# Performance work log

Hardware: AMD Instinct MI355X
Metric: run time of the kernel (lower is better)

## Reference

```python
import jax, jax.numpy as jnp
import numpy as np

TEMPERATURE = 1.0
K = 30
N_CELLS = 200000
LATENT = 256
BATCH = 8192

def setup_inputs() -> dict:
    key = jax.random.key(0)
    k1, k2, k3, k4 = jax.random.split(key, 4)
    z_all = jax.random.normal(k1, (N_CELLS, LATENT), dtype=jnp.float32)
    pre_knn_indices = jax.random.randint(k2, (N_CELLS, K), 0, N_CELLS, dtype=jnp.int64)
    cell_indices = jax.random.randint(k3, (BATCH,), 0, N_CELLS, dtype=jnp.int64)
    neg_indices = jax.random.randint(k4, (BATCH, K), 0, N_CELLS, dtype=jnp.int64)
    return {"z_all": z_all, "pre_knn_indices": pre_knn_indices,
            "cell_indices": cell_indices, "neg_indices": neg_indices}

def reference(z_all, pre_knn_indices, cell_indices, neg_indices):
    # z_all: (N, D); pre_knn_indices: (N, K); cell_indices: (B,); neg_indices: (B, K)
    z_i = z_all[cell_indices]                       # (B, D)
    nn_idx = pre_knn_indices[cell_indices]          # (B, K)
    z_nn = z_all[nn_idx]                            # (B, K, D)
    z_neg = z_all[neg_indices]                      # (B, K, D)
    d_nn = jnp.linalg.norm(z_nn - z_i[:, None, :], axis=-1)    # (B, K)
    d_neg = jnp.linalg.norm(z_neg - z_i[:, None, :], axis=-1)  # (B, K)
    all_dist = jnp.concatenate([d_nn, d_neg], axis=1)          # (B, 2K)
    soft_prob = jax.nn.softmax(-all_dist / TEMPERATURE, axis=1)
    soft_np = soft_prob[:, :K].sum(axis=1)                     # (B,)
    losses = -jnp.log(soft_np + 1e-8)
    return losses.mean()
```

## Files before the change

kernel.cpp:

```cpp
#include <hip/hip_runtime.h>
#include <math.h>

#define BATCH  8192
#define KNEI   30
#define LATENT 256
#define NDIST  60

__global__ __launch_bounds__(256) void softnp_dist_kernel(
    const float* __restrict__ z_all,
    const int* __restrict__ knn,
    const int* __restrict__ cell,
    const int* __restrict__ neg,
    float* __restrict__ losses)
{
    const int b    = blockIdx.x;
    const int tid  = threadIdx.x;
    const int wave = tid >> 6;
    const int lane = tid & 63;

    __shared__ float zi[LATENT];
    __shared__ float dist[NDIST + 4];

    const int ci = cell[b];

    zi[tid] = z_all[(size_t)ci * LATENT + tid];
    __syncthreads();

    const float4 zv = *reinterpret_cast<const float4*>(&zi[lane * 4]);

    for (int k = wave; k < NDIST; k += 4) {
        int idx;
        if (k < KNEI) idx = knn[(size_t)ci * KNEI + k];
        else          idx = neg[(size_t)b * KNEI + (k - KNEI)];

        const float4 v = reinterpret_cast<const float4*>(z_all + (size_t)idx * LATENT)[lane];
        const float dx = v.x - zv.x;
        const float dy = v.y - zv.y;
        const float dz = v.z - zv.z;
        const float dw = v.w - zv.w;
        float s = dx * dx + dy * dy + dz * dz + dw * dw;

        #pragma unroll
        for (int off = 32; off > 0; off >>= 1)
            s += __shfl_xor(s, off, 64);

        if (lane == 0) dist[k] = sqrtf(s);
    }
    __syncthreads();

    if (wave == 0) {
        const float sc = (lane < NDIST) ? -dist[lane] : -INFINITY;

        float m = sc;
        #pragma unroll
        for (int off = 32; off > 0; off >>= 1)
            m = fmaxf(m, __shfl_xor(m, off, 64));

        const float e = (lane < NDIST) ? expf(sc - m) : 0.0f;
        float tot = e;
        float top = (lane < KNEI) ? e : 0.0f;
        #pragma unroll
        for (int off = 32; off > 0; off >>= 1) {
            tot += __shfl_xor(tot, off, 64);
            top += __shfl_xor(top, off, 64);
        }

        if (lane == 0)
            losses[b] = -logf(top / tot + 1e-8f);
    }
}

__global__ __launch_bounds__(1024) void softnp_reduce_kernel(
    const float* __restrict__ losses, float* __restrict__ out)
{
    const int tid  = threadIdx.x;
    const int wave = tid >> 6;
    const int lane = tid & 63;

    float s = 0.0f;
    for (int i = tid; i < BATCH; i += 1024)
        s += losses[i];

    #pragma unroll
    for (int off = 32; off > 0; off >>= 1)
        s += __shfl_xor(s, off, 64);

    __shared__ float buf[16];
    if (lane == 0) buf[wave] = s;
    __syncthreads();

    if (tid == 0) {
        float t = 0.0f;
        #pragma unroll
        for (int i = 0; i < 16; ++i) t += buf[i];
        out[0] = t / (float)BATCH;
    }
}

extern "C" void kernel_launch(void* const* d_in, const int* in_sizes, int n_in,
                              void* d_out, int out_size, void* d_ws, size_t ws_size,
                              hipStream_t stream) {
    const float* z_all = (const float*)d_in[0];
    const int*   knn   = (const int*)d_in[1];
    const int*   cell  = (const int*)d_in[2];
    const int*   neg   = (const int*)d_in[3];
    float* out    = (float*)d_out;
    float* losses = (float*)d_ws;

    softnp_dist_kernel<<<BATCH, 256, 0, stream>>>(z_all, knn, cell, neg, losses);
    softnp_reduce_kernel<<<1, 1024, 0, stream>>>(losses, out);
}
```

Before: 82.51 us.

## Invert gather into per-row scatter so each z_all row is read once

Replaces the per-batch gather of 60 neighbor rows with an inverted index. Each referenced cell row collects the (batch, k) pairs that need it through an atomic scatter, then a per-row kernel reads that z_all row once and computes distances against compact copies of the batch rows. This aims to turn the random 491K-row gather into a mostly sequential sweep over z_all with cached batch rows. In exchange it adds three extra launches, atomics, a count-clearing pass and a full 200K-row scan. It also silently drops any pairs past 64 per row.

```diff
diff --git a/kernel.cpp b/kernel.cpp
--- a/kernel.cpp
+++ b/kernel.cpp
@@ -1,76 +1,106 @@
 #include <hip/hip_runtime.h>
 #include <math.h>
 
+#define NCELLS 200000
 #define BATCH  8192
 #define KNEI   30
 #define LATENT 256
 #define NDIST  60
+#define SLOTS  64
 
-__global__ __launch_bounds__(256) void softnp_dist_kernel(
-    const float* __restrict__ z_all,
-    const int* __restrict__ knn,
-    const int* __restrict__ cell,
+__global__ __launch_bounds__(256) void k1_prep(
+    const float* __restrict__ z_all, const int* __restrict__ cell,
+    float* __restrict__ zb, unsigned* __restrict__ cnt)
+{
+    const int blk = blockIdx.x;
+    if (blk < BATCH / 4) {
+        const int wave = threadIdx.x >> 6, lane = threadIdx.x & 63;
+        const int b  = blk * 4 + wave;
+        const int ci = cell[b];
+        const float4 v = reinterpret_cast<const float4*>(z_all + (size_t)ci * LATENT)[lane];
+        reinterpret_cast<float4*>(zb + (size_t)b * LATENT)[lane] = v;
+    } else {
+        const int i = (blk - BATCH / 4) * 256 + threadIdx.x;
+        if (i < NCELLS) cnt[i] = 0u;
+    }
+}
+
+__global__ __launch_bounds__(256) void k2_scatter(
+    const int* __restrict__ knn, const int* __restrict__ cell,
     const int* __restrict__ neg,
-    float* __restrict__ losses)
+    unsigned* __restrict__ cnt, unsigned* __restrict__ inv)
 {
-    const int b    = blockIdx.x;
-    const int tid  = threadIdx.x;
-    const int wave = tid >> 6;
-    const int lane = tid & 63;
+    const int t = blockIdx.x * 256 + threadIdx.x;
+    const int b = t >> 6, k = t & 63;
+    if (k >= NDIST) return;
+    const int idx = (k < KNEI) ? knn[(size_t)cell[b] * KNEI + k]
+                               : neg[(size_t)b * KNEI + (k - KNEI)];
+    const unsigned pos = atomicAdd(&cnt[idx], 1u);
+    if (pos < SLOTS) inv[(size_t)idx * SLOTS + pos] = (unsigned)(b * 64 + k);
+}
 
-    __shared__ float zi[LATENT];
-    __shared__ float dist[NDIST + 4];
+__global__ __launch_bounds__(256) void k3_dist(
+    const float* __restrict__ z_all, const float* __restrict__ zb,
+    const unsigned* __restrict__ cnt, const unsigned* __restrict__ inv,
+    float* __restrict__ dmat)
+{
+    const int wave = threadIdx.x >> 6, lane = threadIdx.x & 63;
+    const int row  = blockIdx.x * 4 + wave;
+    if (row >= NCELLS) return;
 
-    const int ci = cell[b];
+    unsigned n = cnt[row];
+    if (n == 0) return;
+    if (n > SLOTS) n = SLOTS;
 
-    zi[tid] = z_all[(size_t)ci * LATENT + tid];
-    __syncthreads();
+    const float4 zr = reinterpret_cast<const float4*>(z_all + (size_t)row * LATENT)[lane];
 
-    const float4 zv = *reinterpret_cast<const float4*>(&zi[lane * 4]);
-
-    for (int k = wave; k < NDIST; k += 4) {
-        int idx;
-        if (k < KNEI) idx = knn[(size_t)ci * KNEI + k];
-        else          idx = neg[(size_t)b * KNEI + (k - KNEI)];
-
-        const float4 v = reinterpret_cast<const float4*>(z_all + (size_t)idx * LATENT)[lane];
-        const float dx = v.x - zv.x;
-        const float dy = v.y - zv.y;
-        const float dz = v.z - zv.z;
-        const float dw = v.w - zv.w;
+    for (unsigned r = 0; r < n; ++r) {
+        const unsigned pid = inv[(size_t)row * SLOTS + r];
+        const int b = pid >> 6, k = pid & 63;
+        const float4 v = reinterpret_cast<const float4*>(zb + (size_t)b * LATENT)[lane];
+        const float dx = v.x - zr.x;
+        const float dy = v.y - zr.y;
+        const float dz = v.z - zr.z;
+        const float dw = v.w - zr.w;
         float s = dx * dx + dy * dy + dz * dz + dw * dw;
 
         #pragma unroll
         for (int off = 32; off > 0; off >>= 1)
             s += __shfl_xor(s, off, 64);
 
-        if (lane == 0) dist[k] = sqrtf(s);
-    }
-    __syncthreads();
-
-    if (wave == 0) {
-        const float sc = (lane < NDIST) ? -dist[lane] : -INFINITY;
-
-        float m = sc;
-        #pragma unroll
-        for (int off = 32; off > 0; off >>= 1)
-            m = fmaxf(m, __shfl_xor(m, off, 64));
-
-        const float e = (lane < NDIST) ? expf(sc - m) : 0.0f;
-        float tot = e;
-        float top = (lane < KNEI) ? e : 0.0f;
-        #pragma unroll
-        for (int off = 32; off > 0; off >>= 1) {
-            tot += __shfl_xor(tot, off, 64);
-            top += __shfl_xor(top, off, 64);
-        }
-
-        if (lane == 0)
-            losses[b] = -logf(top / tot + 1e-8f);
+        if (lane == 0) dmat[(size_t)b * 64 + k] = sqrtf(s);
     }
 }
 
-__global__ __launch_bounds__(1024) void softnp_reduce_kernel(
+__global__ __launch_bounds__(256) void k4_softmax(
+    const float* __restrict__ dmat, float* __restrict__ losses)
+{
+    const int wave = threadIdx.x >> 6, lane = threadIdx.x & 63;
+    const int b = blockIdx.x * 4 + wave;
+
+    const bool act = (lane < KNEI) || (lane >= 32 && lane < 32 + KNEI);
+    const int  k   = (lane < 32) ? lane : lane - 2;
+    const float sc = act ? -dmat[(size_t)b * 64 + k] : -INFINITY;
+
+    float m = sc;
+    #pragma unroll
+    for (int off = 32; off > 0; off >>= 1)
+        m = fmaxf(m, __shfl_xor(m, off, 64));
+
+    const float e = act ? expf(sc - m) : 0.0f;
+    float tot = e;
+    float top = (lane < KNEI) ? e : 0.0f;
+    #pragma unroll
+    for (int off = 32; off > 0; off >>= 1) {
+        tot += __shfl_xor(tot, off, 64);
+        top += __shfl_xor(top, off, 64);
+    }
+
+    if (lane == 0)
+        losses[b] = -logf(top / tot + 1e-8f);
+}
+
+__global__ __launch_bounds__(1024) void k5_reduce(
     const float* __restrict__ losses, float* __restrict__ out)
 {
     const int tid  = threadIdx.x;
@@ -104,9 +134,19 @@
     const int*   knn   = (const int*)d_in[1];
     const int*   cell  = (const int*)d_in[2];
     const int*   neg   = (const int*)d_in[3];
-    float* out    = (float*)d_out;
-    float* losses = (float*)d_ws;
+    float* out = (float*)d_out;
 
-    softnp_dist_kernel<<<BATCH, 256, 0, stream>>>(z_all, knn, cell, neg, losses);
-    softnp_reduce_kernel<<<1, 1024, 0, stream>>>(losses, out);
+    char* ws = (char*)d_ws;
+    float*    zb     = (float*)(ws);
+    unsigned* cnt    = (unsigned*)(ws + (8u << 20));
+    unsigned* inv    = (unsigned*)(ws + (16u << 20));
+    float*    dmat   = (float*)(ws + (72u << 20));
+    float*    losses = (float*)(ws + (80u << 20));
+
+    const int k1_grid = BATCH / 4 + (NCELLS + 255) / 256;
+    k1_prep   <<<k1_grid,            256, 0, stream>>>(z_all, cell, zb, cnt);
+    k2_scatter<<<BATCH * 64 / 256,   256, 0, stream>>>(knn, cell, neg, cnt, inv);
+    k3_dist   <<<(NCELLS + 3) / 4,   256, 0, stream>>>(z_all, zb, cnt, inv, dmat);
+    k4_softmax<<<BATCH / 4,          256, 0, stream>>>(dmat, losses);
+    k5_reduce <<<1,                 1024, 0, stream>>>(losses, out);
 }
```

After: 151.2 us. 1.83x slower.
